# Optimization experiments

Hardware: AMD Instinct MI355X
Metric: run time of the kernel (lower is better)

## Reference

```python
import jax, jax.numpy as jnp
import numpy as np

NH = 8          # num_heads (init kwarg)
NUM_GROUPS = 32
EPS = 1e-5


def setup_inputs() -> dict:
    key = jax.random.key(0)
    ks = jax.random.split(key, 4)
    B, C, H, W = 2, 512, 64, 64
    x = jax.random.normal(ks[0], (B, C, H, W), dtype=jnp.float32)
    qkv_w = jax.random.normal(ks[1], (3 * C, C), dtype=jnp.float32) * (1.0 / np.sqrt(C))
    proj_w = jax.random.normal(ks[2], (C, C), dtype=jnp.float32) * (1.0 / np.sqrt(C))
    proj_b = jax.random.normal(ks[3], (C,), dtype=jnp.float32) * 0.02
    gn_w = jnp.ones((C,), dtype=jnp.float32)
    gn_b = jnp.zeros((C,), dtype=jnp.float32)
    return {"x": x, "qkv_w": qkv_w, "proj_w": proj_w, "proj_b": proj_b,
            "gn_w": gn_w, "gn_b": gn_b}


def _group_norm(x, gamma, beta):
    B, C, H, W = x.shape
    xg = x.reshape(B, NUM_GROUPS, C // NUM_GROUPS, H, W)
    mean = xg.mean(axis=(2, 3, 4), keepdims=True)
    var = xg.var(axis=(2, 3, 4), keepdims=True)
    xg = (xg - mean) * jax.lax.rsqrt(var + EPS)
    x = xg.reshape(B, C, H, W)
    return x * gamma[None, :, None, None] + beta[None, :, None, None]


def reference(x, qkv_w, proj_w, proj_b, gn_w, gn_b):
    B, C, H, W = x.shape
    h = _group_norm(x, gn_w, gn_b)
    # 1x1 conv == channel matmul
    qkv = jnp.einsum('oc,bchw->bohw', qkv_w, h)  # [B, 3C, H, W]
    # faithful legacy reshape: per-head contiguous [q,k,v] blocks of 3*C//NH channels
    qkv = qkv.reshape(B * NH, 3 * C // NH, H * W)
    q, k, v = jnp.split(qkv, 3, axis=1)          # each [B*NH, C//NH, HW]
    scale = 1.0 / np.sqrt(np.sqrt(C // NH))
    attn = jnp.einsum('bci,bcj->bij', q * scale, k * scale)  # [B*NH, HW, HW]
    attn = jax.nn.softmax(attn, axis=-1)
    hout = jnp.einsum('bij,bcj->bci', attn, v)   # [B*NH, C//NH, HW]
    hout = hout.reshape(B, C, H, W)
    hout = jnp.einsum('oc,bchw->bohw', proj_w, hout) + proj_b[None, :, None, None]
    return x + hout
```

## Files before the change

kernel.cpp:

```cpp
#include <hip/hip_runtime.h>
#include <math.h>

typedef __attribute__((ext_vector_type(8))) short short8;
typedef __attribute__((ext_vector_type(4))) short short4v;
typedef __attribute__((ext_vector_type(4))) float floatx4;
typedef __attribute__((ext_vector_type(16))) float floatx16;

__device__ __forceinline__ unsigned short f2bf(float f) {
  union { float f; unsigned int u; } v; v.f = f;
  unsigned int r = v.u + 0x7fffu + ((v.u >> 16) & 1u);
  return (unsigned short)(r >> 16);
}

__device__ __forceinline__ float bf2f(unsigned short h) {
  union { unsigned int u; float f; } v; v.u = ((unsigned int)h) << 16;
  return v.f;
}

__device__ __forceinline__ unsigned int pack2(unsigned short a, unsigned short b) {
  return (unsigned int)a | ((unsigned int)b << 16);
}

__device__ __forceinline__ unsigned int rbits(float f) {
  union { float f; unsigned int u; } v; v.f = f;
  return v.u + 0x8000u;
}

__device__ __forceinline__ float fast_exp2(float x) {
#if __has_builtin(__builtin_amdgcn_exp2f)
  return __builtin_amdgcn_exp2f(x);
#else
  return exp2f(x);
#endif
}

__device__ __forceinline__ void async16(const unsigned short* gp, unsigned short* lp) {
  __builtin_amdgcn_global_load_lds(
      (__attribute__((address_space(1))) void*)(gp),
      (__attribute__((address_space(3))) void*)(lp), 16, 0, 0);
}

__global__ void gn_stats(const float* __restrict__ x, float* __restrict__ stats) {
  int bg = blockIdx.x;
  const float4* p = (const float4*)(x + (size_t)bg * 65536);
  float s = 0.f, ss = 0.f;
  for (int i = threadIdx.x; i < 16384; i += 256) {
    float4 v = p[i];
    s  += v.x + v.y + v.z + v.w;
    ss += v.x*v.x + v.y*v.y + v.z*v.z + v.w*v.w;
  }
  #pragma unroll
  for (int off = 32; off >= 1; off >>= 1) {
    s  += __shfl_xor(s,  off, 64);
    ss += __shfl_xor(ss, off, 64);
  }
  __shared__ float red[2][4];
  int wv = threadIdx.x >> 6;
  if ((threadIdx.x & 63) == 0) { red[0][wv] = s; red[1][wv] = ss; }
  __syncthreads();
  if (threadIdx.x == 0) {
    s  = red[0][0] + red[0][1] + red[0][2] + red[0][3];
    ss = red[1][0] + red[1][1] + red[1][2] + red[1][3];
    float mean = s * (1.f/65536.f);
    float var  = ss * (1.f/65536.f) - mean*mean;
    stats[2*bg]   = mean;
    stats[2*bg+1] = rsqrtf(var + 1e-5f);
  }
}

__global__ void gn_apply_t(const float* __restrict__ x, const float* __restrict__ stats,
                           const float* __restrict__ gw, const float* __restrict__ gb,
                           unsigned short* __restrict__ h_t) {
  __shared__ __align__(16) unsigned short tile[64][72];
  const int b = blockIdx.z, c0 = blockIdx.y * 64, hw0 = blockIdx.x * 64;
  const int t = threadIdx.x;
  {
    const int cl = t >> 2;
    const int hs = (t & 3) * 16;
    const int c  = c0 + cl;
    const int g  = c >> 4;
    const float mean = stats[2*(b*32 + g)];
    const float rstd = stats[2*(b*32 + g) + 1];
    const float w  = gw[c] * rstd;
    const float bb = gb[c] - mean * w;
    const float4* src = (const float4*)(x + ((size_t)(b*512 + c))*4096 + hw0 + hs);
    #pragma unroll
    for (int i = 0; i < 4; i++) {
      float4 vv = src[i];
      unsigned short* d = &tile[cl][hs + i*4];
      d[0] = f2bf(vv.x*w + bb); d[1] = f2bf(vv.y*w + bb);
      d[2] = f2bf(vv.z*w + bb); d[3] = f2bf(vv.w*w + bb);
    }
  }
  __syncthreads();
  {
    const int hwl = t >> 2;
    const int cs  = (t & 3) * 16;
    uint4 w0, w1;
    w0.x = pack2(tile[cs+ 0][hwl], tile[cs+ 1][hwl]);
    w0.y = pack2(tile[cs+ 2][hwl], tile[cs+ 3][hwl]);
    w0.z = pack2(tile[cs+ 4][hwl], tile[cs+ 5][hwl]);
    w0.w = pack2(tile[cs+ 6][hwl], tile[cs+ 7][hwl]);
    w1.x = pack2(tile[cs+ 8][hwl], tile[cs+ 9][hwl]);
    w1.y = pack2(tile[cs+10][hwl], tile[cs+11][hwl]);
    w1.z = pack2(tile[cs+12][hwl], tile[cs+13][hwl]);
    w1.w = pack2(tile[cs+14][hwl], tile[cs+15][hwl]);
    unsigned short* dst = h_t + ((size_t)(b*4096 + hw0 + hwl))*512 + c0 + cs;
    *(uint4*)dst       = w0;
    *(uint4*)(dst + 8) = w1;
  }
}

__global__ void castw2(const float* __restrict__ sa, unsigned short* __restrict__ da, int n4a,
                       const float* __restrict__ sb, unsigned short* __restrict__ db) {
  int i = blockIdx.x * 256 + threadIdx.x;
  const float* s; unsigned short* d;
  if (i < n4a) { s = sa; d = da; }
  else { i -= n4a; s = sb; d = db; }
  float4 vv = ((const float4*)s)[i];
  uint2 o;
  o.x = pack2(f2bf(vv.x), f2bf(vv.y));
  o.y = pack2(f2bf(vv.z), f2bf(vv.w));
  ((uint2*)d)[i] = o;
}

template <int MODE>
__global__ __launch_bounds__(256, 2)
void gemm_bt(const unsigned short* __restrict__ A,
             const unsigned short* __restrict__ Bt,
             unsigned short* __restrict__ q_t,
             unsigned short* __restrict__ k_t,
             unsigned short* __restrict__ v_,
             float* __restrict__ outp,
             const float* __restrict__ xres,
             const float* __restrict__ pbias) {
  __shared__ __align__(16) unsigned short As[128*32];
  __shared__ __align__(16) unsigned short Bs[128*32];
  const int b   = blockIdx.z;
  const int n0  = blockIdx.x * 128;
  const int o0  = blockIdx.y * 128;
  const int tid = threadIdx.x;
  const int wave = tid >> 6, lane = tid & 63;
  const int wr = wave >> 1, wc = wave & 1;
  const int fm = lane & 15, fq = lane >> 4;
  const int srow = lane >> 2, scol = (lane & 3) * 8;

  const unsigned short* Ab = A + (size_t)o0 * 512;
  const unsigned short* Bb = Bt + ((size_t)b*4096 + n0) * 512;

  bool vsw[4];
  #pragma unroll
  for (int fr = 0; fr < 4; fr++) {
    const int ob = o0 + wr*64 + fr*16;
    vsw[fr] = (MODE == 0) && ((ob % 192) >> 6) == 2;
  }

  floatx4 acc[4][4];
  #pragma unroll
  for (int i = 0; i < 4; i++)
    #pragma unroll
    for (int j = 0; j < 4; j++) acc[i][j] = (floatx4){0.f,0.f,0.f,0.f};

  for (int k0 = 0; k0 < 512; k0 += 32) {
    __syncthreads();
    #pragma unroll
    for (int cc = 0; cc < 2; cc++) {
      int ch = wave*2 + cc;
      async16(Ab + (size_t)(ch*16 + srow)*512 + k0 + scol, &As[ch*512]);
      async16(Bb + (size_t)(ch*16 + srow)*512 + k0 + scol, &Bs[ch*512]);
    }
    __syncthreads();
    short8 af[4], bf[4];
    #pragma unroll
    for (int f = 0; f < 4; f++) {
      af[f] = *(const short8*)&As[(wr*64 + f*16 + fm)*32 + fq*8];
      bf[f] = *(const short8*)&Bs[(wc*64 + f*16 + fm)*32 + fq*8];
    }
    #pragma unroll
    for (int fr = 0; fr < 4; fr++) {
      if (vsw[fr]) {
        #pragma unroll
        for (int fc = 0; fc < 4; fc++)
          acc[fr][fc] = __builtin_amdgcn_mfma_f32_16x16x32_bf16(bf[fc], af[fr], acc[fr][fc], 0, 0, 0);
      } else {
        #pragma unroll
        for (int fc = 0; fc < 4; fc++)
          acc[fr][fc] = __builtin_amdgcn_mfma_f32_16x16x32_bf16(af[fr], bf[fc], acc[fr][fc], 0, 0, 0);
      }
    }
  }

  if (MODE == 0) {
    #pragma unroll
    for (int fr = 0; fr < 4; fr++) {
      const int ob     = o0 + wr*64 + fr*16;
      const int head   = ob / 192;
      const int rem    = ob % 192;
      const int region = rem >> 6;
      const int bhh    = b*8 + head;
      #pragma unroll
      for (int fc = 0; fc < 4; fc++) {
        if (region == 0) {
          const int i = n0 + wc*64 + fc*16 + fm;
          const int dsub = (rem & 63) + fq*4;
          unsigned short t4[4];
          #pragma unroll
          for (int r = 0; r < 4; r++) t4[r] = f2bf(acc[fr][fc][r] * 0.18033688f);
          uint2 o; o.x = pack2(t4[0], t4[1]); o.y = pack2(t4[2], t4[3]);
          *(uint2*)&q_t[((size_t)bhh*4096 + i)*64 + dsub] = o;
        } else if (region == 1) {
          const int i = n0 + wc*64 + fc*16 + fm;
          const int dsub = (rem & 63) + fq*4;
          unsigned short t4[4];
          #pragma unroll
          for (int r = 0; r < 4; r++) t4[r] = f2bf(acc[fr][fc][r]);
          uint2 o; o.x = pack2(t4[0], t4[1]); o.y = pack2(t4[2], t4[3]);
          *(uint2*)&k_t[((size_t)bhh*4096 + i)*64 + dsub] = o;
        } else {
          const int dsub = (rem & 63) + fm;
          const int tok0 = n0 + wc*64 + fc*16 + fq*4;
          unsigned short t4[4];
          #pragma unroll
          for (int r = 0; r < 4; r++) t4[r] = f2bf(acc[fr][fc][r]);
          uint2 o; o.x = pack2(t4[0], t4[1]); o.y = pack2(t4[2], t4[3]);
          *(uint2*)&v_[((size_t)bhh*64 + dsub)*4096 + tok0] = o;
        }
      }
    }
  } else {
    #pragma unroll
    for (int fr = 0; fr < 4; fr++)
      #pragma unroll
      for (int fc = 0; fc < 4; fc++) {
        const int i = n0 + wc*64 + fc*16 + fm;
        #pragma unroll
        for (int r = 0; r < 4; r++) {
          const int o = o0 + wr*64 + fr*16 + fq*4 + r;
          const size_t idx = ((size_t)b*512 + o)*4096 + i;
          outp[idx] = xres[idx] + pbias[o] + acc[fr][fc][r];
        }
      }
  }
}

template <int SPLIT>
__global__ __launch_bounds__(256, 4)
void attn_kernel(const unsigned short* __restrict__ q_t,
                 const unsigned short* __restrict__ k_t,
                 const unsigned short* __restrict__ v_,
                 unsigned short* __restrict__ hout_t,
                 unsigned short* __restrict__ o_part,
                 float* __restrict__ l_part) {
  __shared__ __align__(16) unsigned short Ks[2][64*72];
  __shared__ __align__(16) unsigned short Vs[2][64*72];

  const int bh  = blockIdx.x;
  const int q0  = blockIdx.y * 128;
  const int js  = SPLIT ? blockIdx.z : 0;
  const int nit = SPLIT ? 32 : 64;
  const int jbase = js * 2048;
  const int tid = threadIdx.x;
  const int wave = tid >> 6, lane = tid & 63;
  const int ln = lane & 31, h = lane >> 5;

  short8 qf[4];
  {
    const unsigned short* qrow = q_t + ((size_t)bh*4096 + q0 + wave*32 + ln)*64;
    #pragma unroll
    for (int kc = 0; kc < 4; kc++)
      qf[kc] = *(const short8*)(qrow + kc*16 + h*8);
  }

  const floatx16 z16 = {0.f,0.f,0.f,0.f,0.f,0.f,0.f,0.f,
                        0.f,0.f,0.f,0.f,0.f,0.f,0.f,0.f};
  floatx16 o_acc[2];
  o_acc[0] = z16; o_acc[1] = z16;
  float l = 0.f;

  const int sr = tid >> 3;
  const int sc = (tid & 7) * 8;
  const int c  = tid & 7;
  const int vpos = ((c >> 2) * 32) + ((c & 3) * 4);
  const unsigned short* kbase = k_t + (size_t)bh*262144;
  const unsigned short* vbase = v_  + (size_t)bh*262144;

  uint4 kr0 = *(const uint4*)&kbase[(size_t)(jbase + sr)*64 + sc];
  uint4 kr1 = *(const uint4*)&kbase[(size_t)(jbase + sr + 32)*64 + sc];
  uint4 vr0 = *(const uint4*)&vbase[(size_t)sr*4096 + jbase + sc];
  uint4 vr1 = *(const uint4*)&vbase[(size_t)(sr+32)*4096 + jbase + sc];

  for (int it = 0; it < nit; it++) {
    unsigned short* Kc = Ks[it & 1];
    unsigned short* Vc = Vs[it & 1];
    *(uint4*)&Kc[sr*72 + sc]      = kr0;
    *(uint4*)&Kc[(sr+32)*72 + sc] = kr1;
    *(uint2*)&Vc[sr*72 + vpos]           = *(const uint2*)&vr0;
    *(uint2*)&Vc[sr*72 + vpos + 16]      = *((const uint2*)&vr0 + 1);
    *(uint2*)&Vc[(sr+32)*72 + vpos]      = *(const uint2*)&vr1;
    *(uint2*)&Vc[(sr+32)*72 + vpos + 16] = *((const uint2*)&vr1 + 1);
    __syncthreads();

    {
      const int jn = jbase + (((it + 1) & (nit - 1)) * 64);
      kr0 = *(const uint4*)&kbase[(size_t)(jn + sr)*64 + sc];
      kr1 = *(const uint4*)&kbase[(size_t)(jn + sr + 32)*64 + sc];
      vr0 = *(const uint4*)&vbase[(size_t)sr*4096 + jn + sc];
      vr1 = *(const uint4*)&vbase[(size_t)(sr+32)*4096 + jn + sc];
    }

    #pragma unroll
    for (int mj = 0; mj < 2; mj++) {
      floatx16 st;
      {
        short8 kA = *(const short8*)&Kc[(mj*32 + ln)*72 + h*8];
        st = __builtin_amdgcn_mfma_f32_32x32x16_bf16(kA, qf[0], z16, 0, 0, 0);
      }
      #pragma unroll
      for (int kc = 1; kc < 4; kc++) {
        short8 kA = *(const short8*)&Kc[(mj*32 + ln)*72 + kc*16 + h*8];
        st = __builtin_amdgcn_mfma_f32_32x32x16_bf16(kA, qf[kc], st, 0, 0, 0);
      }

      unsigned pk[8];
      #pragma unroll
      for (int rp = 0; rp < 8; rp++) {
        float p0 = fast_exp2(st[2*rp]);
        float p1 = fast_exp2(st[2*rp + 1]);
        l += p0 + p1;
        pk[rp] = __builtin_amdgcn_perm(rbits(p1), rbits(p0), 0x07060302u);
      }

      #pragma unroll
      for (int t2 = 0; t2 < 2; t2++) {
        union { unsigned u[2]; short4v s; } a0, a1;
        a0.u[0] = pk[4*t2];     a0.u[1] = pk[4*t2 + 1];
        a1.u[0] = pk[4*t2 + 2]; a1.u[1] = pk[4*t2 + 3];
        #pragma unroll
        for (int dn = 0; dn < 2; dn++) {
          short8 vv = *(const short8*)&Vc[(dn*32 + ln)*72 + mj*32 + h*16 + t2*8];
          short4v vlo = __builtin_shufflevector(vv, vv, 0, 1, 2, 3);
          short4v vhi = __builtin_shufflevector(vv, vv, 4, 5, 6, 7);
          o_acc[dn] = __builtin_amdgcn_mfma_f32_32x32x8bf16_1k(a0.s, vlo, o_acc[dn], 0, 0, 0);
          o_acc[dn] = __builtin_amdgcn_mfma_f32_32x32x8bf16_1k(a1.s, vhi, o_acc[dn], 0, 0, 0);
        }
      }
    }
  }

  l += __shfl_xor(l, 32, 64);

  if (SPLIT) {
    unsigned short* op = o_part + (((size_t)(js*16 + bh)*4096 + q0 + wave*32) * 64);
    #pragma unroll
    for (int r = 0; r < 16; r++) {
      const int il = (r & 3) + 8*(r >> 2) + 4*h;
      op[(size_t)il*64 + ln]      = f2bf(o_acc[0][r]);
      op[(size_t)il*64 + 32 + ln] = f2bf(o_acc[1][r]);
    }
    if (lane < 32)
      l_part[(size_t)(js*16 + bh)*4096 + q0 + wave*32 + lane] = l;
  } else {
    const float linv = 1.f / l;
    const int bb = bh >> 3;
    const int cb = (bh & 7) * 64;
    #pragma unroll
    for (int r = 0; r < 16; r++) {
      const int il = (r & 3) + 8*(r >> 2) + 4*h;
      const float inv = __shfl(linv, il, 64);
      const int i = q0 + wave*32 + il;
      unsigned short* dst = &hout_t[((size_t)bb*4096 + i)*512 + cb + ln];
      dst[0]  = f2bf(o_acc[0][r] * inv);
      dst[32] = f2bf(o_acc[1][r] * inv);
    }
  }
}

__global__ void attn_combine(const unsigned short* __restrict__ o_part,
                             const float* __restrict__ l_part,
                             unsigned short* __restrict__ hout_t) {
  const int bh = blockIdx.x;
  const int i0 = blockIdx.y * 64;
  const int t  = threadIdx.x;
  const int d4 = (t & 15) * 4;
  const int il = t >> 4;
  const int bb = bh >> 3;
  const int cb = (bh & 7) * 64;
  const size_t JS = (size_t)16 * 4096 * 64;
  #pragma unroll
  for (int p = 0; p < 4; p++) {
    const int i = i0 + p*16 + il;
    const size_t ob = ((size_t)bh*4096 + i)*64 + d4;
    uint2 a = *(const uint2*)&o_part[ob];
    uint2 b = *(const uint2*)&o_part[ob + JS];
    const size_t lb = (size_t)bh*4096 + i;
    const float inv = 1.f / (l_part[lb] + l_part[lb + 65536]);
    float o0 = (bf2f((unsigned short)(a.x & 0xffff)) + bf2f((unsigned short)(b.x & 0xffff))) * inv;
    float o1 = (bf2f((unsigned short)(a.x >> 16))    + bf2f((unsigned short)(b.x >> 16)))    * inv;
    float o2 = (bf2f((unsigned short)(a.y & 0xffff)) + bf2f((unsigned short)(b.y & 0xffff))) * inv;
    float o3 = (bf2f((unsigned short)(a.y >> 16))    + bf2f((unsigned short)(b.y >> 16)))    * inv;
    uint2 w;
    w.x = pack2(f2bf(o0), f2bf(o1));
    w.y = pack2(f2bf(o2), f2bf(o3));
    *(uint2*)&hout_t[((size_t)bb*4096 + i)*512 + cb + d4] = w;
  }
}

extern "C" void kernel_launch(void* const* d_in, const int* in_sizes, int n_in,
                              void* d_out, int out_size, void* d_ws, size_t ws_size,
                              hipStream_t stream) {
  (void)in_sizes; (void)n_in; (void)out_size;
  const float* x      = (const float*)d_in[0];
  const float* qkv_w  = (const float*)d_in[1];
  const float* proj_w = (const float*)d_in[2];
  const float* proj_b = (const float*)d_in[3];
  const float* gn_w   = (const float*)d_in[4];
  const float* gn_b   = (const float*)d_in[5];
  float* out = (float*)d_out;

  char* ws = (char*)d_ws;
  unsigned short* h_t   = (unsigned short*)(ws);
  unsigned short* q_t   = (unsigned short*)(ws + ((size_t)8  << 20));
  unsigned short* k_t   = (unsigned short*)(ws + ((size_t)16 << 20));
  unsigned short* v_    = (unsigned short*)(ws + ((size_t)24 << 20));
  unsigned short* wqkv  = (unsigned short*)(ws + ((size_t)32 << 20));
  unsigned short* wproj = (unsigned short*)(ws + ((size_t)34 << 20));
  float* stats          = (float*)(ws + ((size_t)35 << 20));
  unsigned short* o_part = (unsigned short*)(ws + ((size_t)36 << 20));
  float* l_part          = (float*)(ws + ((size_t)52 << 20));
  unsigned short* hout_t = h_t;

  const bool split = ws_size >= (((size_t)52 << 20) + ((size_t)1 << 19));

  gn_stats<<<dim3(64), dim3(256), 0, stream>>>(x, stats);
  gn_apply_t<<<dim3(64, 8, 2), dim3(256), 0, stream>>>(x, stats, gn_w, gn_b, h_t);
  castw2<<<dim3(1024), dim3(256), 0, stream>>>(qkv_w, wqkv, 196608, proj_w, wproj);
  gemm_bt<0><<<dim3(32, 12, 2), dim3(256), 0, stream>>>(wqkv, h_t, q_t, k_t, v_,
                                                        nullptr, nullptr, nullptr);
  if (split) {
    attn_kernel<1><<<dim3(16, 32, 2), dim3(256), 0, stream>>>(q_t, k_t, v_, nullptr,
                                                              o_part, l_part);
    attn_combine<<<dim3(16, 64), dim3(256), 0, stream>>>(o_part, l_part, hout_t);
  } else {
    attn_kernel<0><<<dim3(16, 32), dim3(256), 0, stream>>>(q_t, k_t, v_, hout_t,
                                                           nullptr, nullptr);
  }
  gemm_bt<1><<<dim3(32, 4, 2), dim3(256), 0, stream>>>(wproj, hout_t,
                                                       nullptr, nullptr, nullptr,
                                                       out, x, proj_b);
}
```

Before: 232.9 us.

## Load K fragments directly to registers in attention, merge setup kernels, retile proj GEMM

The attention kernel stops staging K in shared memory. Each lane loads its K MFMA fragments straight from global memory into registers and prefetches the next tile, which removes the K LDS writes and reads and halves LDS use. Occupancy bounds drop from 4 to 3 blocks because register pressure rises. Separately, gn_stats and the weight cast are merged into one launch, and the projection GEMM uses 64-row tiles so it launches twice as many blocks. Direct global K loads are uncoalesced per lane and may raise memory latency.

```diff
diff --git a/kernel.cpp b/kernel.cpp
--- a/kernel.cpp
+++ b/kernel.cpp
@@ -24,6 +24,10 @@
 __device__ __forceinline__ unsigned int rbits(float f) {
   union { float f; unsigned int u; } v; v.f = f;
   return v.u + 0x8000u;
+}
+
+__device__ __forceinline__ short8 as_short8(uint4 u) {
+  union { uint4 u; short8 s; } v; v.u = u; return v.s;
 }
 
 __device__ __forceinline__ float fast_exp2(float x) {
@@ -40,31 +44,45 @@
       (__attribute__((address_space(3))) void*)(lp), 16, 0, 0);
 }
 
-__global__ void gn_stats(const float* __restrict__ x, float* __restrict__ stats) {
-  int bg = blockIdx.x;
-  const float4* p = (const float4*)(x + (size_t)bg * 65536);
-  float s = 0.f, ss = 0.f;
-  for (int i = threadIdx.x; i < 16384; i += 256) {
-    float4 v = p[i];
-    s  += v.x + v.y + v.z + v.w;
-    ss += v.x*v.x + v.y*v.y + v.z*v.z + v.w*v.w;
-  }
-  #pragma unroll
-  for (int off = 32; off >= 1; off >>= 1) {
-    s  += __shfl_xor(s,  off, 64);
-    ss += __shfl_xor(ss, off, 64);
-  }
-  __shared__ float red[2][4];
-  int wv = threadIdx.x >> 6;
-  if ((threadIdx.x & 63) == 0) { red[0][wv] = s; red[1][wv] = ss; }
-  __syncthreads();
-  if (threadIdx.x == 0) {
-    s  = red[0][0] + red[0][1] + red[0][2] + red[0][3];
-    ss = red[1][0] + red[1][1] + red[1][2] + red[1][3];
-    float mean = s * (1.f/65536.f);
-    float var  = ss * (1.f/65536.f) - mean*mean;
-    stats[2*bg]   = mean;
-    stats[2*bg+1] = rsqrtf(var + 1e-5f);
+__global__ void setup_kernel(const float* __restrict__ x, float* __restrict__ stats,
+                             const float* __restrict__ qkv_w, unsigned short* __restrict__ wqkv,
+                             const float* __restrict__ proj_w, unsigned short* __restrict__ wproj) {
+  if (blockIdx.x < 64) {
+    int bg = blockIdx.x;
+    const float4* p = (const float4*)(x + (size_t)bg * 65536);
+    float s = 0.f, ss = 0.f;
+    for (int i = threadIdx.x; i < 16384; i += 256) {
+      float4 v = p[i];
+      s  += v.x + v.y + v.z + v.w;
+      ss += v.x*v.x + v.y*v.y + v.z*v.z + v.w*v.w;
+    }
+    #pragma unroll
+    for (int off = 32; off >= 1; off >>= 1) {
+      s  += __shfl_xor(s,  off, 64);
+      ss += __shfl_xor(ss, off, 64);
+    }
+    __shared__ float red[2][4];
+    int wv = threadIdx.x >> 6;
+    if ((threadIdx.x & 63) == 0) { red[0][wv] = s; red[1][wv] = ss; }
+    __syncthreads();
+    if (threadIdx.x == 0) {
+      s  = red[0][0] + red[0][1] + red[0][2] + red[0][3];
+      ss = red[1][0] + red[1][1] + red[1][2] + red[1][3];
+      float mean = s * (1.f/65536.f);
+      float var  = ss * (1.f/65536.f) - mean*mean;
+      stats[2*bg]   = mean;
+      stats[2*bg+1] = rsqrtf(var + 1e-5f);
+    }
+  } else {
+    int i = (blockIdx.x - 64) * 256 + threadIdx.x;
+    const float* s; unsigned short* d;
+    if (i < 196608) { s = qkv_w; d = wqkv; }
+    else { i -= 196608; s = proj_w; d = wproj; }
+    float4 vv = ((const float4*)s)[i];
+    uint2 o;
+    o.x = pack2(f2bf(vv.x), f2bf(vv.y));
+    o.y = pack2(f2bf(vv.z), f2bf(vv.w));
+    ((uint2*)d)[i] = o;
   }
 }
 
@@ -111,29 +129,12 @@
   }
 }
 
-__global__ void castw2(const float* __restrict__ sa, unsigned short* __restrict__ da, int n4a,
-                       const float* __restrict__ sb, unsigned short* __restrict__ db) {
-  int i = blockIdx.x * 256 + threadIdx.x;
-  const float* s; unsigned short* d;
-  if (i < n4a) { s = sa; d = da; }
-  else { i -= n4a; s = sb; d = db; }
-  float4 vv = ((const float4*)s)[i];
-  uint2 o;
-  o.x = pack2(f2bf(vv.x), f2bf(vv.y));
-  o.y = pack2(f2bf(vv.z), f2bf(vv.w));
-  ((uint2*)d)[i] = o;
-}
-
-template <int MODE>
 __global__ __launch_bounds__(256, 2)
-void gemm_bt(const unsigned short* __restrict__ A,
-             const unsigned short* __restrict__ Bt,
-             unsigned short* __restrict__ q_t,
-             unsigned short* __restrict__ k_t,
-             unsigned short* __restrict__ v_,
-             float* __restrict__ outp,
-             const float* __restrict__ xres,
-             const float* __restrict__ pbias) {
+void qkv_gemm(const unsigned short* __restrict__ A,
+              const unsigned short* __restrict__ Bt,
+              unsigned short* __restrict__ q_t,
+              unsigned short* __restrict__ k_t,
+              unsigned short* __restrict__ v_) {
   __shared__ __align__(16) unsigned short As[128*32];
   __shared__ __align__(16) unsigned short Bs[128*32];
   const int b   = blockIdx.z;
@@ -152,7 +153,7 @@
   #pragma unroll
   for (int fr = 0; fr < 4; fr++) {
     const int ob = o0 + wr*64 + fr*16;
-    vsw[fr] = (MODE == 0) && ((ob % 192) >> 6) == 2;
+    vsw[fr] = ((ob % 192) >> 6) == 2;
   }
 
   floatx4 acc[4][4];
@@ -190,68 +191,115 @@
     }
   }
 
-  if (MODE == 0) {
-    #pragma unroll
-    for (int fr = 0; fr < 4; fr++) {
-      const int ob     = o0 + wr*64 + fr*16;
-      const int head   = ob / 192;
-      const int rem    = ob % 192;
-      const int region = rem >> 6;
-      const int bhh    = b*8 + head;
+  #pragma unroll
+  for (int fr = 0; fr < 4; fr++) {
+    const int ob     = o0 + wr*64 + fr*16;
+    const int head   = ob / 192;
+    const int rem    = ob % 192;
+    const int region = rem >> 6;
+    const int bhh    = b*8 + head;
+    #pragma unroll
+    for (int fc = 0; fc < 4; fc++) {
+      if (region == 0) {
+        const int i = n0 + wc*64 + fc*16 + fm;
+        const int dsub = (rem & 63) + fq*4;
+        unsigned short t4[4];
+        #pragma unroll
+        for (int r = 0; r < 4; r++) t4[r] = f2bf(acc[fr][fc][r] * 0.18033688f);
+        uint2 o; o.x = pack2(t4[0], t4[1]); o.y = pack2(t4[2], t4[3]);
+        *(uint2*)&q_t[((size_t)bhh*4096 + i)*64 + dsub] = o;
+      } else if (region == 1) {
+        const int i = n0 + wc*64 + fc*16 + fm;
+        const int dsub = (rem & 63) + fq*4;
+        unsigned short t4[4];
+        #pragma unroll
+        for (int r = 0; r < 4; r++) t4[r] = f2bf(acc[fr][fc][r]);
+        uint2 o; o.x = pack2(t4[0], t4[1]); o.y = pack2(t4[2], t4[3]);
+        *(uint2*)&k_t[((size_t)bhh*4096 + i)*64 + dsub] = o;
+      } else {
+        const int dsub = (rem & 63) + fm;
+        const int tok0 = n0 + wc*64 + fc*16 + fq*4;
+        unsigned short t4[4];
+        #pragma unroll
+        for (int r = 0; r < 4; r++) t4[r] = f2bf(acc[fr][fc][r]);
+        uint2 o; o.x = pack2(t4[0], t4[1]); o.y = pack2(t4[2], t4[3]);
+        *(uint2*)&v_[((size_t)bhh*64 + dsub)*4096 + tok0] = o;
+      }
+    }
+  }
+}
+
+__global__ __launch_bounds__(256, 2)
+void proj_gemm(const unsigned short* __restrict__ A,
+               const unsigned short* __restrict__ Bt,
+               float* __restrict__ outp,
+               const float* __restrict__ xres,
+               const float* __restrict__ pbias) {
+  __shared__ __align__(16) unsigned short As[64*32];
+  __shared__ __align__(16) unsigned short Bs[128*32];
+  const int b   = blockIdx.z;
+  const int n0  = blockIdx.x * 128;
+  const int o0  = blockIdx.y * 64;
+  const int tid = threadIdx.x;
+  const int wave = tid >> 6, lane = tid & 63;
+  const int wr = wave >> 1, wc = wave & 1;
+  const int fm = lane & 15, fq = lane >> 4;
+  const int srow = lane >> 2, scol = (lane & 3) * 8;
+
+  const unsigned short* Ab = A + (size_t)o0 * 512;
+  const unsigned short* Bb = Bt + ((size_t)b*4096 + n0) * 512;
+
+  floatx4 acc[2][4];
+  #pragma unroll
+  for (int i = 0; i < 2; i++)
+    #pragma unroll
+    for (int j = 0; j < 4; j++) acc[i][j] = (floatx4){0.f,0.f,0.f,0.f};
+
+  for (int k0 = 0; k0 < 512; k0 += 32) {
+    __syncthreads();
+    async16(Ab + (size_t)(wave*16 + srow)*512 + k0 + scol, &As[wave*512]);
+    #pragma unroll
+    for (int cc = 0; cc < 2; cc++) {
+      int ch = wave*2 + cc;
+      async16(Bb + (size_t)(ch*16 + srow)*512 + k0 + scol, &Bs[ch*512]);
+    }
+    __syncthreads();
+    short8 af[2], bf[4];
+    #pragma unroll
+    for (int f = 0; f < 2; f++)
+      af[f] = *(const short8*)&As[(wr*32 + f*16 + fm)*32 + fq*8];
+    #pragma unroll
+    for (int f = 0; f < 4; f++)
+      bf[f] = *(const short8*)&Bs[(wc*64 + f*16 + fm)*32 + fq*8];
+    #pragma unroll
+    for (int fr = 0; fr < 2; fr++)
       #pragma unroll
-      for (int fc = 0; fc < 4; fc++) {
-        if (region == 0) {
-          const int i = n0 + wc*64 + fc*16 + fm;
-          const int dsub = (rem & 63) + fq*4;
-          unsigned short t4[4];
-          #pragma unroll
-          for (int r = 0; r < 4; r++) t4[r] = f2bf(acc[fr][fc][r] * 0.18033688f);
-          uint2 o; o.x = pack2(t4[0], t4[1]); o.y = pack2(t4[2], t4[3]);
-          *(uint2*)&q_t[((size_t)bhh*4096 + i)*64 + dsub] = o;
-        } else if (region == 1) {
-          const int i = n0 + wc*64 + fc*16 + fm;
-          const int dsub = (rem & 63) + fq*4;
-          unsigned short t4[4];
-          #pragma unroll
-          for (int r = 0; r < 4; r++) t4[r] = f2bf(acc[fr][fc][r]);
-          uint2 o; o.x = pack2(t4[0], t4[1]); o.y = pack2(t4[2], t4[3]);
-          *(uint2*)&k_t[((size_t)bhh*4096 + i)*64 + dsub] = o;
-        } else {
-          const int dsub = (rem & 63) + fm;
-          const int tok0 = n0 + wc*64 + fc*16 + fq*4;
-          unsigned short t4[4];
-          #pragma unroll
-          for (int r = 0; r < 4; r++) t4[r] = f2bf(acc[fr][fc][r]);
-          uint2 o; o.x = pack2(t4[0], t4[1]); o.y = pack2(t4[2], t4[3]);
-          *(uint2*)&v_[((size_t)bhh*64 + dsub)*4096 + tok0] = o;
-        }
-      }
-    }
-  } else {
-    #pragma unroll
-    for (int fr = 0; fr < 4; fr++)
+      for (int fc = 0; fc < 4; fc++)
+        acc[fr][fc] = __builtin_amdgcn_mfma_f32_16x16x32_bf16(af[fr], bf[fc], acc[fr][fc], 0, 0, 0);
+  }
+
+  #pragma unroll
+  for (int fr = 0; fr < 2; fr++)
+    #pragma unroll
+    for (int fc = 0; fc < 4; fc++) {
+      const int i = n0 + wc*64 + fc*16 + fm;
       #pragma unroll
-      for (int fc = 0; fc < 4; fc++) {
-        const int i = n0 + wc*64 + fc*16 + fm;
-        #pragma unroll
-        for (int r = 0; r < 4; r++) {
-          const int o = o0 + wr*64 + fr*16 + fq*4 + r;
-          const size_t idx = ((size_t)b*512 + o)*4096 + i;
-          outp[idx] = xres[idx] + pbias[o] + acc[fr][fc][r];
-        }
-      }
-  }
+      for (int r = 0; r < 4; r++) {
+        const int o = o0 + wr*32 + fr*16 + fq*4 + r;
+        const size_t idx = ((size_t)b*512 + o)*4096 + i;
+        outp[idx] = xres[idx] + pbias[o] + acc[fr][fc][r];
+      }
+    }
 }
 
 template <int SPLIT>
-__global__ __launch_bounds__(256, 4)
+__global__ __launch_bounds__(256, 3)
 void attn_kernel(const unsigned short* __restrict__ q_t,
                  const unsigned short* __restrict__ k_t,
                  const unsigned short* __restrict__ v_,
                  unsigned short* __restrict__ hout_t,
                  unsigned short* __restrict__ o_part,
                  float* __restrict__ l_part) {
-  __shared__ __align__(16) unsigned short Ks[2][64*72];
   __shared__ __align__(16) unsigned short Vs[2][64*72];
 
   const int bh  = blockIdx.x;
@@ -279,47 +327,52 @@
 
   const int sr = tid >> 3;
   const int sc = (tid & 7) * 8;
-  const int c  = tid & 7;
-  const int vpos = ((c >> 2) * 32) + ((c & 3) * 4);
-  const unsigned short* kbase = k_t + (size_t)bh*262144;
-  const unsigned short* vbase = v_  + (size_t)bh*262144;
-
-  uint4 kr0 = *(const uint4*)&kbase[(size_t)(jbase + sr)*64 + sc];
-  uint4 kr1 = *(const uint4*)&kbase[(size_t)(jbase + sr + 32)*64 + sc];
+  const int cch = tid & 7;
+  const int vpos = ((cch >> 2) * 32) + ((cch & 3) * 4);
+  const unsigned short* vbase = v_ + (size_t)bh*262144;
+  const unsigned short* kflane = k_t + (size_t)bh*262144 + (size_t)ln*64 + h*8;
+
   uint4 vr0 = *(const uint4*)&vbase[(size_t)sr*4096 + jbase + sc];
   uint4 vr1 = *(const uint4*)&vbase[(size_t)(sr+32)*4096 + jbase + sc];
+  uint4 ka[4], kb[4];
+  {
+    const unsigned short* kp = kflane + (size_t)jbase*64;
+    #pragma unroll
+    for (int kc = 0; kc < 4; kc++) ka[kc] = *(const uint4*)(kp + kc*16);
+  }
 
   for (int it = 0; it < nit; it++) {
-    unsigned short* Kc = Ks[it & 1];
-    unsigned short* Vc = Vs[it & 1];
-    *(uint4*)&Kc[sr*72 + sc]      = kr0;
-    *(uint4*)&Kc[(sr+32)*72 + sc] = kr1;
+    unsigned short* Vc = (unsigned short*)Vs[it & 1];
     *(uint2*)&Vc[sr*72 + vpos]           = *(const uint2*)&vr0;
     *(uint2*)&Vc[sr*72 + vpos + 16]      = *((const uint2*)&vr0 + 1);
     *(uint2*)&Vc[(sr+32)*72 + vpos]      = *(const uint2*)&vr1;
     *(uint2*)&Vc[(sr+32)*72 + vpos + 16] = *((const uint2*)&vr1 + 1);
     __syncthreads();
 
-    {
-      const int jn = jbase + (((it + 1) & (nit - 1)) * 64);
-      kr0 = *(const uint4*)&kbase[(size_t)(jn + sr)*64 + sc];
-      kr1 = *(const uint4*)&kbase[(size_t)(jn + sr + 32)*64 + sc];
-      vr0 = *(const uint4*)&vbase[(size_t)sr*4096 + jn + sc];
-      vr1 = *(const uint4*)&vbase[(size_t)(sr+32)*4096 + jn + sc];
-    }
+    const int jn = jbase + (((it + 1) & (nit - 1)) * 64);
+    vr0 = *(const uint4*)&vbase[(size_t)sr*4096 + jn + sc];
+    vr1 = *(const uint4*)&vbase[(size_t)(sr+32)*4096 + jn + sc];
+
+    const unsigned short* kcur = kflane + ((size_t)jbase + (size_t)it*64)*64;
+    const unsigned short* knxt = kflane + (size_t)jn*64;
 
     #pragma unroll
     for (int mj = 0; mj < 2; mj++) {
+      if (mj == 0) {
+        #pragma unroll
+        for (int kc = 0; kc < 4; kc++) kb[kc] = *(const uint4*)(kcur + 2048 + kc*16);
+      } else {
+        #pragma unroll
+        for (int kc = 0; kc < 4; kc++) ka[kc] = *(const uint4*)(knxt + kc*16);
+      }
+
       floatx16 st;
-      {
-        short8 kA = *(const short8*)&Kc[(mj*32 + ln)*72 + h*8];
-        st = __builtin_amdgcn_mfma_f32_32x32x16_bf16(kA, qf[0], z16, 0, 0, 0);
-      }
+      st = __builtin_amdgcn_mfma_f32_32x32x16_bf16(
+          as_short8(mj == 0 ? ka[0] : kb[0]), qf[0], z16, 0, 0, 0);
       #pragma unroll
-      for (int kc = 1; kc < 4; kc++) {
-        short8 kA = *(const short8*)&Kc[(mj*32 + ln)*72 + kc*16 + h*8];
-        st = __builtin_amdgcn_mfma_f32_32x32x16_bf16(kA, qf[kc], st, 0, 0, 0);
-      }
+      for (int kc = 1; kc < 4; kc++)
+        st = __builtin_amdgcn_mfma_f32_32x32x16_bf16(
+            as_short8(mj == 0 ? ka[kc] : kb[kc]), qf[kc], st, 0, 0, 0);
 
       unsigned pk[8];
       #pragma unroll
@@ -431,11 +484,9 @@
 
   const bool split = ws_size >= (((size_t)52 << 20) + ((size_t)1 << 19));
 
-  gn_stats<<<dim3(64), dim3(256), 0, stream>>>(x, stats);
+  setup_kernel<<<dim3(1088), dim3(256), 0, stream>>>(x, stats, qkv_w, wqkv, proj_w, wproj);
   gn_apply_t<<<dim3(64, 8, 2), dim3(256), 0, stream>>>(x, stats, gn_w, gn_b, h_t);
-  castw2<<<dim3(1024), dim3(256), 0, stream>>>(qkv_w, wqkv, 196608, proj_w, wproj);
-  gemm_bt<0><<<dim3(32, 12, 2), dim3(256), 0, stream>>>(wqkv, h_t, q_t, k_t, v_,
-                                                        nullptr, nullptr, nullptr);
+  qkv_gemm<<<dim3(32, 12, 2), dim3(256), 0, stream>>>(wqkv, h_t, q_t, k_t, v_);
   if (split) {
     attn_kernel<1><<<dim3(16, 32, 2), dim3(256), 0, stream>>>(q_t, k_t, v_, nullptr,
                                                               o_part, l_part);
@@ -444,7 +495,5 @@
     attn_kernel<0><<<dim3(16, 32), dim3(256), 0, stream>>>(q_t, k_t, v_, hout_t,
                                                            nullptr, nullptr);
   }
-  gemm_bt<1><<<dim3(32, 4, 2), dim3(256), 0, stream>>>(wproj, hout_t,
-                                                       nullptr, nullptr, nullptr,
-                                                       out, x, proj_b);
-}
+  proj_gemm<<<dim3(32, 8, 2), dim3(256), 0, stream>>>(wproj, hout_t, out, x, proj_b);
+}
```

New measurement: 281.2 us. +20.7%, slower.
